# Kernel optimization log

Hardware: AMD Instinct MI355X
Metric: run time of the kernel (lower is better)

## Reference

```python
import jax, jax.numpy as jnp
import numpy as np

B, F, S, P, E, H = 64, 32, 512, 96, 8, 2048
TOP_K = 2
ALPHA = 10.0
ENT_EPS = 1e-8
CV_EPS = 1e-10


def setup_inputs() -> dict:
    key = jax.random.key(0)
    ks = jax.random.split(key, 8)
    s = 0.02
    return {
        "x": jax.random.normal(ks[0], (B, F, S), dtype=jnp.float32),
        "time_embedding": jax.random.normal(ks[1], (B, F, S), dtype=jnp.float32),
        "Wg": jax.random.normal(ks[2], (S, E), dtype=jnp.float32) * s,
        "bg": jnp.zeros((E,), dtype=jnp.float32),
        "W1": jax.random.normal(ks[3], (E, S, H), dtype=jnp.float32) * s,
        "b1": jnp.zeros((E, H), dtype=jnp.float32),
        "W2": jax.random.normal(ks[4], (E, H, P), dtype=jnp.float32) * s,
        "b2": jnp.zeros((E, P), dtype=jnp.float32),
    }


def _gates(tf, Wg, bg):
    # tf: [F, B, S] -> logits [F, B, E]
    logits = jnp.einsum('fbs,se->fbe', tf, Wg) + bg
    # kthvalue(x, E - top_k + 1) = (E - top_k)-th entry (0-based) of ascending sort = k-th largest
    kth = jnp.sort(logits, axis=-1)[..., E - TOP_K]  # [F, B]
    mask = logits < kth[..., None]
    sm = jax.nn.softmax(logits, axis=-1)
    dec = jnp.where(mask, ALPHA * jnp.log(sm + 1.0), ALPHA * (jnp.exp(sm) - 1.0))
    return jax.nn.softmax(dec, axis=-1)  # [F, B, E]


def reference(x, time_embedding, Wg, bg, W1, b1, W2, b2):
    xf = jnp.transpose(x, (1, 0, 2))               # [F, B, S]
    tf = jnp.transpose(time_embedding, (1, 0, 2))  # [F, B, S]
    gates = _gates(tf, Wg, bg)                     # [F, B, E]

    # all experts on all features (eval mode: dropout = identity)
    h = jax.nn.gelu(jnp.einsum('fbs,esh->febh', xf, W1) + b1[None, :, None, :], approximate=False)
    eo = jnp.einsum('febh,ehp->febp', h, W2) + b2[None, :, None, :]  # [F, E, B, P]
    out = jnp.einsum('fbe,febp->fbp', gates, eo)   # gated weighted sum
    output = jnp.transpose(out, (1, 0, 2))         # [B, F, P]

    # selector loss: cv_squared of importance = gates.sum(batch) expanded over pred_len
    gsum = gates.sum(axis=1)                       # [F, E]
    imp = jnp.broadcast_to(gsum[..., None], (F, E, P)).reshape(F, E * P)
    cv = jnp.var(imp, axis=1, ddof=1) / (jnp.mean(imp, axis=1) ** 2 + CV_EPS)
    selector_loss = jnp.sum(cv)                    # loss_coef = 1.0

    # entropy loss: importance1 = gates.mean(batch) expanded over pred_len
    gmean = gates.mean(axis=1)                     # [F, E]
    imp1 = jnp.broadcast_to(gmean[..., None], (F, E, P))
    entropy_loss = jnp.sum((-imp1 * jnp.log(imp1 + ENT_EPS)).mean(axis=(1, 2)))

    return output, selector_loss, entropy_loss
```

## Files before the change

### kernel.cpp

```cpp
#include <hip/hip_runtime.h>
#include <math.h>

#define B_ 64
#define F_ 32
#define S_ 512
#define P_ 96
#define E_ 8
#define H_ 2048
#define M_ 2048

#define BM 128
#define BH 128
#define BK 64
#define ZSPLIT 4
#define HPZ (H_ / ZSPLIT)
#define NHT (HPZ / BH)
#define NKC (S_ / BK)
#define HPITCH 136

typedef __bf16 bf16x8 __attribute__((ext_vector_type(8)));
typedef __bf16 bf16x4 __attribute__((ext_vector_type(4)));
typedef float f32x4 __attribute__((ext_vector_type(4)));

#define MFMA16(a, b, c) __builtin_amdgcn_mfma_f32_16x16x32_bf16((a), (b), (c), 0, 0, 0)

#define GLL16(gp, lp) __builtin_amdgcn_global_load_lds(                     \
    (const __attribute__((address_space(1))) void*)(gp),                    \
    (__attribute__((address_space(3))) void*)(lp), 16, 0, 0)

__device__ __forceinline__ float fast_gelu(float x) {
  float e = __builtin_amdgcn_exp2f(-2.45546696f * x);
  return x * __builtin_amdgcn_rcpf(1.0f + e);
}

#define PREP_GRID 3584

__global__ __launch_bounds__(256) void k_prep(const float* __restrict__ x,
                                              const float* __restrict__ te,
                                              const float* __restrict__ Wg,
                                              const float* __restrict__ bg,
                                              const float* __restrict__ W1,
                                              const float* __restrict__ W2,
                                              __bf16* __restrict__ xbf,
                                              __bf16* __restrict__ w1t,
                                              __bf16* __restrict__ w2t,
                                              float* __restrict__ gates) {
  __shared__ float tile[64 * 65];
  const int blk = blockIdx.x;
  const int tid = threadIdx.x;

  if (blk < 2048) {
    int e = blk >> 8, tt = blk & 255;
    int si = tt >> 5, hi = tt & 31;
    const float* src = W1 + (size_t)e * S_ * H_ + (size_t)(si * 64) * H_ + hi * 64;
    {
      int row = tid >> 2;
      int cb = (tid & 3) * 16;
#pragma unroll
      for (int k = 0; k < 4; ++k) {
        f32x4 v = *(const f32x4*)(src + (size_t)row * H_ + cb + k * 4);
#pragma unroll
        for (int u = 0; u < 4; ++u) tile[row * 65 + cb + k * 4 + u] = v[u];
      }
    }
    __syncthreads();
    {
      int h = tid >> 2;
      int sb = (tid & 3) * 16;
      __bf16* dst = w1t + (size_t)e * H_ * S_ + (size_t)(hi * 64 + h) * S_ + si * 64 + sb;
      bf16x8 o0, o1;
#pragma unroll
      for (int k = 0; k < 8; ++k) o0[k] = (__bf16)tile[(sb + k) * 65 + h];
#pragma unroll
      for (int k = 0; k < 8; ++k) o1[k] = (__bf16)tile[(sb + 8 + k) * 65 + h];
      *(bf16x8*)dst = o0;
      *(bf16x8*)(dst + 8) = o1;
    }
    return;
  }
  if (blk < 2560) {
    int t = blk - 2048;
    int e = t >> 6, hi = (t >> 1) & 31, ph = t & 1;
    const float* src = W2 + (size_t)e * H_ * P_ + (size_t)(hi * 64) * P_ + ph * 48;
    {
      int h = tid & 63;
      int seg = tid >> 6;
#pragma unroll
      for (int k = 0; k < 3; ++k) {
        f32x4 v = *(const f32x4*)(src + (size_t)h * P_ + seg * 12 + k * 4);
#pragma unroll
        for (int u = 0; u < 4; ++u) tile[h * 49 + seg * 12 + k * 4 + u] = v[u];
      }
    }
    __syncthreads();
    if (tid < 192) {
      int p = tid >> 2;
      int hb = (tid & 3) * 16;
      __bf16* dst = w2t + (size_t)e * P_ * H_ + (size_t)(ph * 48 + p) * H_ + hi * 64 + hb;
      bf16x8 o0, o1;
#pragma unroll
      for (int k = 0; k < 8; ++k) o0[k] = (__bf16)tile[(hb + k) * 49 + p];
#pragma unroll
      for (int k = 0; k < 8; ++k) o1[k] = (__bf16)tile[(hb + 8 + k) * 49 + p];
      *(bf16x8*)dst = o0;
      *(bf16x8*)(dst + 8) = o1;
    }
    return;
  }
  if (blk < 3072) {
    size_t i = (size_t)(blk - 2560) * 2048 + (size_t)tid * 8;
#pragma unroll
    for (int k = 0; k < 2; ++k) {
      f32x4 v = *(const f32x4*)(x + i + k * 4);
      bf16x4 o = {(__bf16)v[0], (__bf16)v[1], (__bf16)v[2], (__bf16)v[3]};
      *(bf16x4*)(xbf + i + k * 4) = o;
    }
    return;
  }
  int wave = tid >> 6, lane = tid & 63;
  int m = (blk - 3072) * 4 + wave;
  const float* trow = te + (size_t)m * S_;
  float acc[E_];
#pragma unroll
  for (int e = 0; e < E_; ++e) acc[e] = 0.f;
  for (int s = lane; s < S_; s += 64) {
    float t = trow[s];
    const f32x4* wgr = (const f32x4*)(Wg + s * E_);
    f32x4 a = wgr[0], b = wgr[1];
    acc[0] += t * a[0]; acc[1] += t * a[1]; acc[2] += t * a[2]; acc[3] += t * a[3];
    acc[4] += t * b[0]; acc[5] += t * b[1]; acc[6] += t * b[2]; acc[7] += t * b[3];
  }
#pragma unroll
  for (int e = 0; e < E_; ++e) {
#pragma unroll
    for (int off = 32; off > 0; off >>= 1) acc[e] += __shfl_xor(acc[e], off, 64);
  }
  if (lane == 0) {
    float lg[E_];
    float m1 = -3.4e38f, m2 = -3.4e38f;
#pragma unroll
    for (int e = 0; e < E_; ++e) {
      float v = acc[e] + bg[e];
      lg[e] = v;
      if (v > m1) { m2 = m1; m1 = v; }
      else if (v > m2) { m2 = v; }
    }
    float den = 0.f, sm[E_];
#pragma unroll
    for (int e = 0; e < E_; ++e) { sm[e] = expf(lg[e] - m1); den += sm[e]; }
    float inv = 1.f / den;
    float dmax = -3.4e38f, dec[E_];
#pragma unroll
    for (int e = 0; e < E_; ++e) {
      float p = sm[e] * inv;
      float d = (lg[e] < m2) ? (10.f * logf(p + 1.f)) : (10.f * (expf(p) - 1.f));
      dec[e] = d;
      dmax = fmaxf(dmax, d);
    }
    float dden = 0.f;
#pragma unroll
    for (int e = 0; e < E_; ++e) { dec[e] = expf(dec[e] - dmax); dden += dec[e]; }
    float dinv = 1.f / dden;
#pragma unroll
    for (int e = 0; e < E_; ++e) gates[m * E_ + e] = dec[e] * dinv;
  }
}

__global__ __launch_bounds__(256, 2) void k_experts(
    const __bf16* __restrict__ xbf,
    const __bf16* __restrict__ w1t,
    const __bf16* __restrict__ w2t,
    const float* __restrict__ b1,
    const float* __restrict__ b2,
    const float* __restrict__ gates,
    float* __restrict__ out)
{
  __shared__ __align__(16) __bf16 W1s[BH * BK];
  __shared__ __align__(16) __bf16 Xs[BM * BK];
  __shared__ __align__(16) __bf16 Hs[BM * HPITCH];

  const int tid = threadIdx.x;

  if (blockIdx.z == ZSPLIT) {
    if (blockIdx.x != 0 || blockIdx.y != 0) return;
    float* gsum = (float*)&Hs[0];
    float* cvs  = gsum + F_ * E_;
    float* ents = cvs + F_;
    int f = tid >> 3, e = tid & 7;
    float s = 0.f;
    for (int b = 0; b < B_; ++b) s += gates[(size_t)(b * F_ + f) * E_ + e];
    gsum[f * E_ + e] = s;
    __syncthreads();
    if (tid < F_) {
      float mean = 0.f;
#pragma unroll
      for (int k = 0; k < E_; ++k) mean += gsum[tid * E_ + k];
      mean *= (1.f / E_);
      float ss = 0.f;
#pragma unroll
      for (int k = 0; k < E_; ++k) { float d = gsum[tid * E_ + k] - mean; ss += d * d; }
      float var = (float)P_ * ss / (float)(E_ * P_ - 1);
      cvs[tid] = var / (mean * mean + 1e-10f);
      float ent = 0.f;
#pragma unroll
      for (int k = 0; k < E_; ++k) { float g = gsum[tid * E_ + k] * (1.f / B_); ent += -g * logf(g + 1e-8f); }
      ents[tid] = ent * (1.f / E_);
    }
    __syncthreads();
    if (tid == 0) {
      float a = 0.f, b = 0.f;
      for (int k = 0; k < F_; ++k) { a += cvs[k]; b += ents[k]; }
      out[(size_t)M_ * P_ + 0] = a;
      out[(size_t)M_ * P_ + 1] = b;
    }
    return;
  }

  const int wave = tid >> 6, lane = tid & 63;
  const int l15 = lane & 15, quad = lane >> 4;
  const int e = blockIdx.x;
  const int m0 = blockIdx.y * BM;
  const int hz = blockIdx.z * HPZ;

  const int sg = lane & 7;
  const int srl = lane >> 3;
  const int gcol = ((sg ^ srl) * 8);

  const __bf16* xg = xbf + (size_t)(m0 + wave * 8 + srl) * S_ + gcol;
  const __bf16* w1base = w1t + ((size_t)e * H_ + hz + wave * 8 + srl) * S_ + gcol;
  const __bf16* w2z = w2t + (size_t)e * P_ * H_ + hz;

  const int hq = (wave >> 1) * 64;
  const int mq = (wave & 1) * 64;
  const int w32 = wave * 32;

  const f32x4 fz = {0.f, 0.f, 0.f, 0.f};
  f32x4 acc2[2][6];
#pragma unroll
  for (int rt = 0; rt < 2; ++rt)
#pragma unroll
    for (int j = 0; j < 6; ++j) acc2[rt][j] = fz;

  for (int ht = 0; ht < NHT; ++ht) {
    const __bf16* w1g = w1base + (size_t)(ht * BH) * S_;
    f32x4 acc1[4][4];
#pragma unroll
    for (int i = 0; i < 4; ++i)
#pragma unroll
      for (int j = 0; j < 4; ++j) acc1[i][j] = fz;

    for (int kc = 0; kc < NKC; ++kc) {
#pragma unroll
      for (int p = 0; p < 4; ++p) {
        GLL16(w1g + (size_t)(p * 32) * S_ + kc * BK, &W1s[(p * 32 + wave * 8) * BK]);
        GLL16(xg  + (size_t)(p * 32) * S_ + kc * BK, &Xs[(p * 32 + wave * 8) * BK]);
      }
      __syncthreads();
#pragma unroll
      for (int kk = 0; kk < 2; ++kk) {
        bf16x8 a[4], b[4];
#pragma unroll
        for (int i = 0; i < 4; ++i) {
          int r = hq + i * 16 + l15;
          int g = kk * 4 + quad;
          a[i] = *(const bf16x8*)&W1s[r * BK + ((g ^ (r & 7)) * 8)];
        }
#pragma unroll
        for (int j = 0; j < 4; ++j) {
          int r = mq + j * 16 + l15;
          int g = kk * 4 + quad;
          b[j] = *(const bf16x8*)&Xs[r * BK + ((g ^ (r & 7)) * 8)];
        }
#pragma unroll
        for (int i = 0; i < 4; ++i)
#pragma unroll
          for (int j = 0; j < 4; ++j)
            acc1[i][j] = MFMA16(a[i], b[j], acc1[i][j]);
      }
      __syncthreads();
    }

    {
      const float* b1w = b1 + (size_t)e * H_ + hz + ht * BH + hq;
#pragma unroll
      for (int i = 0; i < 4; ++i) {
        f32x4 bv = *(const f32x4*)(b1w + i * 16 + quad * 4);
#pragma unroll
        for (int j = 0; j < 4; ++j) {
          bf16x4 hv;
#pragma unroll
          for (int r = 0; r < 4; ++r)
            hv[r] = (__bf16)fast_gelu(acc1[i][j][r] + bv[r]);
          *(bf16x4*)&Hs[(mq + j * 16 + l15) * HPITCH + hq + i * 16 + quad * 4] = hv;
        }
      }
    }
    __syncthreads();

    {
      const __bf16* w2c = w2z + ht * BH;
#pragma unroll
      for (int kk = 0; kk < 4; ++kk) {
        bf16x8 a0 = *(const bf16x8*)&Hs[(w32 + l15) * HPITCH + kk * 32 + quad * 8];
        bf16x8 a1 = *(const bf16x8*)&Hs[(w32 + 16 + l15) * HPITCH + kk * 32 + quad * 8];
#pragma unroll
        for (int j = 0; j < 6; ++j) {
          bf16x8 b = *(const bf16x8*)(w2c + (size_t)(j * 16 + l15) * H_ + kk * 32 + quad * 8);
          acc2[0][j] = MFMA16(a0, b, acc2[0][j]);
          acc2[1][j] = MFMA16(a1, b, acc2[1][j]);
        }
      }
    }
  }

#pragma unroll
  for (int rt = 0; rt < 2; ++rt) {
#pragma unroll
    for (int r = 0; r < 4; ++r) {
      int m = m0 + w32 + rt * 16 + quad * 4 + r;
      float g = gates[m * E_ + e];
#pragma unroll
      for (int j = 0; j < 6; ++j) {
        int col = j * 16 + l15;
        float v = acc2[rt][j][r];
        if (blockIdx.z == 0) v += b2[e * P_ + col];
        atomicAdd(&out[(size_t)m * P_ + col], g * v);
      }
    }
  }
}

extern "C" void kernel_launch(void* const* d_in, const int* in_sizes, int n_in,
                              void* d_out, int out_size, void* d_ws, size_t ws_size,
                              hipStream_t stream) {
  const float* x  = (const float*)d_in[0];
  const float* te = (const float*)d_in[1];
  const float* Wg = (const float*)d_in[2];
  const float* bg = (const float*)d_in[3];
  const float* W1 = (const float*)d_in[4];
  const float* b1 = (const float*)d_in[5];
  const float* W2 = (const float*)d_in[6];
  const float* b2 = (const float*)d_in[7];
  float* out = (float*)d_out;

  char* ws = (char*)d_ws;
  float* gates = (float*)ws;
  __bf16* xbf  = (__bf16*)(ws + 65536);
  __bf16* w1t  = (__bf16*)(ws + 65536 + 2097152);
  __bf16* w2t  = (__bf16*)(ws + 65536 + 2097152 + 16777216);

  hipMemsetAsync(d_out, 0, (size_t)out_size * sizeof(float), stream);
  k_prep<<<PREP_GRID, 256, 0, stream>>>(x, te, Wg, bg, W1, W2, xbf, w1t, w2t, gates);
  k_experts<<<dim3(E_, M_ / BM, ZSPLIT + 1), 256, 0, stream>>>(xbf, w1t, w2t, b1, b2, gates, out);
}
```

Baseline: 194.1 us.

## Double-buffer expert GEMM stages, stage W2 in LDS, fold output zeroing into prep

The expert kernel now uses 512-thread blocks with double-buffered W1/X LDS tiles. The next k-chunk loads while the current one computes, and the second GEMM for the previous h-tile overlaps the first chunk of the next. W2 tiles are staged into swizzled LDS instead of being read directly from global memory, and the H split drops from 4 to 2 to halve atomic traffic. The separate memset is replaced by extra zeroing blocks in the prep kernel, removing one launch. The trade-off is fewer blocks, higher LDS use per block and more serialized h-tiles per block.

```diff
diff --git a/kernel.cpp b/kernel.cpp
--- a/kernel.cpp
+++ b/kernel.cpp
@@ -12,7 +12,7 @@
 #define BM 128
 #define BH 128
 #define BK 64
-#define ZSPLIT 4
+#define ZSPLIT 2
 #define HPZ (H_ / ZSPLIT)
 #define NHT (HPZ / BH)
 #define NKC (S_ / BK)
@@ -33,7 +33,7 @@
   return x * __builtin_amdgcn_rcpf(1.0f + e);
 }
 
-#define PREP_GRID 3584
+#define PREP_GRID 3776
 
 __global__ __launch_bounds__(256) void k_prep(const float* __restrict__ x,
                                               const float* __restrict__ te,
@@ -44,7 +44,8 @@
                                               __bf16* __restrict__ xbf,
                                               __bf16* __restrict__ w1t,
                                               __bf16* __restrict__ w2t,
-                                              float* __restrict__ gates) {
+                                              float* __restrict__ gates,
+                                              float* __restrict__ out) {
   __shared__ float tile[64 * 65];
   const int blk = blockIdx.x;
   const int tid = threadIdx.x;
@@ -117,56 +118,64 @@
     }
     return;
   }
-  int wave = tid >> 6, lane = tid & 63;
-  int m = (blk - 3072) * 4 + wave;
-  const float* trow = te + (size_t)m * S_;
-  float acc[E_];
-#pragma unroll
-  for (int e = 0; e < E_; ++e) acc[e] = 0.f;
-  for (int s = lane; s < S_; s += 64) {
-    float t = trow[s];
-    const f32x4* wgr = (const f32x4*)(Wg + s * E_);
-    f32x4 a = wgr[0], b = wgr[1];
-    acc[0] += t * a[0]; acc[1] += t * a[1]; acc[2] += t * a[2]; acc[3] += t * a[3];
-    acc[4] += t * b[0]; acc[5] += t * b[1]; acc[6] += t * b[2]; acc[7] += t * b[3];
-  }
-#pragma unroll
-  for (int e = 0; e < E_; ++e) {
-#pragma unroll
-    for (int off = 32; off > 0; off >>= 1) acc[e] += __shfl_xor(acc[e], off, 64);
-  }
-  if (lane == 0) {
-    float lg[E_];
-    float m1 = -3.4e38f, m2 = -3.4e38f;
+  if (blk < 3584) {
+    int wave = tid >> 6, lane = tid & 63;
+    int m = (blk - 3072) * 4 + wave;
+    const float* trow = te + (size_t)m * S_;
+    float acc[E_];
+#pragma unroll
+    for (int e = 0; e < E_; ++e) acc[e] = 0.f;
+    for (int s = lane; s < S_; s += 64) {
+      float t = trow[s];
+      const f32x4* wgr = (const f32x4*)(Wg + s * E_);
+      f32x4 a = wgr[0], b = wgr[1];
+      acc[0] += t * a[0]; acc[1] += t * a[1]; acc[2] += t * a[2]; acc[3] += t * a[3];
+      acc[4] += t * b[0]; acc[5] += t * b[1]; acc[6] += t * b[2]; acc[7] += t * b[3];
+    }
 #pragma unroll
     for (int e = 0; e < E_; ++e) {
-      float v = acc[e] + bg[e];
-      lg[e] = v;
-      if (v > m1) { m2 = m1; m1 = v; }
-      else if (v > m2) { m2 = v; }
-    }
-    float den = 0.f, sm[E_];
-#pragma unroll
-    for (int e = 0; e < E_; ++e) { sm[e] = expf(lg[e] - m1); den += sm[e]; }
-    float inv = 1.f / den;
-    float dmax = -3.4e38f, dec[E_];
-#pragma unroll
-    for (int e = 0; e < E_; ++e) {
-      float p = sm[e] * inv;
-      float d = (lg[e] < m2) ? (10.f * logf(p + 1.f)) : (10.f * (expf(p) - 1.f));
-      dec[e] = d;
-      dmax = fmaxf(dmax, d);
-    }
-    float dden = 0.f;
-#pragma unroll
-    for (int e = 0; e < E_; ++e) { dec[e] = expf(dec[e] - dmax); dden += dec[e]; }
-    float dinv = 1.f / dden;
-#pragma unroll
-    for (int e = 0; e < E_; ++e) gates[m * E_ + e] = dec[e] * dinv;
+#pragma unroll
+      for (int off = 32; off > 0; off >>= 1) acc[e] += __shfl_xor(acc[e], off, 64);
+    }
+    if (lane == 0) {
+      float lg[E_];
+      float m1 = -3.4e38f, m2 = -3.4e38f;
+#pragma unroll
+      for (int e = 0; e < E_; ++e) {
+        float v = acc[e] + bg[e];
+        lg[e] = v;
+        if (v > m1) { m2 = m1; m1 = v; }
+        else if (v > m2) { m2 = v; }
+      }
+      float den = 0.f, sm[E_];
+#pragma unroll
+      for (int e = 0; e < E_; ++e) { sm[e] = expf(lg[e] - m1); den += sm[e]; }
+      float inv = 1.f / den;
+      float dmax = -3.4e38f, dec[E_];
+#pragma unroll
+      for (int e = 0; e < E_; ++e) {
+        float p = sm[e] * inv;
+        float d = (lg[e] < m2) ? (10.f * logf(p + 1.f)) : (10.f * (expf(p) - 1.f));
+        dec[e] = d;
+        dmax = fmaxf(dmax, d);
+      }
+      float dden = 0.f;
+#pragma unroll
+      for (int e = 0; e < E_; ++e) { dec[e] = expf(dec[e] - dmax); dden += dec[e]; }
+      float dinv = 1.f / dden;
+#pragma unroll
+      for (int e = 0; e < E_; ++e) gates[m * E_ + e] = dec[e] * dinv;
+    }
+    return;
+  }
+  {
+    size_t i = (size_t)(blk - 3584) * 1024 + (size_t)tid * 4;
+    f32x4 z4 = {0.f, 0.f, 0.f, 0.f};
+    *(f32x4*)(out + i) = z4;
   }
 }
 
-__global__ __launch_bounds__(256, 2) void k_experts(
+__global__ __launch_bounds__(512, 2) void k_experts(
     const __bf16* __restrict__ xbf,
     const __bf16* __restrict__ w1t,
     const __bf16* __restrict__ w2t,
@@ -175,8 +184,9 @@
     const float* __restrict__ gates,
     float* __restrict__ out)
 {
-  __shared__ __align__(16) __bf16 W1s[BH * BK];
-  __shared__ __align__(16) __bf16 Xs[BM * BK];
+  __shared__ __align__(16) __bf16 W1s[2][BH * BK];
+  __shared__ __align__(16) __bf16 Xs[2][BM * BK];
+  __shared__ __align__(16) __bf16 W2s[P_ * BH];
   __shared__ __align__(16) __bf16 Hs[BM * HPITCH];
 
   const int tid = threadIdx.x;
@@ -186,10 +196,12 @@
     float* gsum = (float*)&Hs[0];
     float* cvs  = gsum + F_ * E_;
     float* ents = cvs + F_;
-    int f = tid >> 3, e = tid & 7;
-    float s = 0.f;
-    for (int b = 0; b < B_; ++b) s += gates[(size_t)(b * F_ + f) * E_ + e];
-    gsum[f * E_ + e] = s;
+    if (tid < 256) {
+      int f = tid >> 3, ee = tid & 7;
+      float s = 0.f;
+      for (int b = 0; b < B_; ++b) s += gates[(size_t)(b * F_ + f) * E_ + ee];
+      gsum[f * E_ + ee] = s;
+    }
     __syncthreads();
     if (tid < F_) {
       float mean = 0.f;
@@ -226,106 +238,127 @@
   const int srl = lane >> 3;
   const int gcol = ((sg ^ srl) * 8);
 
-  const __bf16* xg = xbf + (size_t)(m0 + wave * 8 + srl) * S_ + gcol;
-  const __bf16* w1base = w1t + ((size_t)e * H_ + hz + wave * 8 + srl) * S_ + gcol;
+  const __bf16* w1base = w1t + ((size_t)e * H_ + hz + wave * 16 + srl) * S_ + gcol;
+  const __bf16* xg = xbf + (size_t)(m0 + wave * 16 + srl) * S_ + gcol;
   const __bf16* w2z = w2t + (size_t)e * P_ * H_ + hz;
 
-  const int hq = (wave >> 1) * 64;
-  const int mq = (wave & 1) * 64;
-  const int w32 = wave * 32;
+  const int hq = (wave & 1) * 64;
+  const int mq = (wave >> 1) * 32;
+  const int w16 = wave * 16;
 
   const f32x4 fz = {0.f, 0.f, 0.f, 0.f};
-  f32x4 acc2[2][6];
-#pragma unroll
-  for (int rt = 0; rt < 2; ++rt)
-#pragma unroll
-    for (int j = 0; j < 6; ++j) acc2[rt][j] = fz;
+  f32x4 acc1[4][2];
+  f32x4 acc2[6];
+#pragma unroll
+  for (int j = 0; j < 6; ++j) acc2[j] = fz;
+
+  auto STAGE = [&](int ht_, int kc_, int b) {
+    const __bf16* w1p = w1base + (size_t)(ht_ * BH) * S_ + kc_ * BK;
+    const __bf16* xp  = xg + kc_ * BK;
+#pragma unroll
+    for (int p = 0; p < 2; ++p) {
+      GLL16(w1p + (size_t)(p * 8) * S_, &W1s[b][(wave * 16 + p * 8) * BK]);
+      GLL16(xp  + (size_t)(p * 8) * S_, &Xs[b][(wave * 16 + p * 8) * BK]);
+    }
+  };
+
+  auto STAGEW2 = [&](int ht_) {
+#pragma unroll
+    for (int p = 0; p < 3; ++p) {
+      int r2 = wave * 12 + p * 4 + quad;
+      GLL16(w2z + (size_t)r2 * H_ + ht_ * BH + ((l15 ^ (r2 & 7)) * 8),
+            &W2s[(wave * 12 + p * 4) * BH]);
+    }
+  };
+
+  auto COMPUTE = [&](int b) {
+#pragma unroll
+    for (int kk = 0; kk < 2; ++kk) {
+      bf16x8 af[4], bx[2];
+#pragma unroll
+      for (int i = 0; i < 4; ++i) {
+        int r = hq + i * 16 + l15;
+        af[i] = *(const bf16x8*)&W1s[b][r * BK + (((kk * 4 + quad) ^ (r & 7)) * 8)];
+      }
+#pragma unroll
+      for (int j = 0; j < 2; ++j) {
+        int r = mq + j * 16 + l15;
+        bx[j] = *(const bf16x8*)&Xs[b][r * BK + (((kk * 4 + quad) ^ (r & 7)) * 8)];
+      }
+#pragma unroll
+      for (int i = 0; i < 4; ++i)
+#pragma unroll
+        for (int j = 0; j < 2; ++j)
+          acc1[i][j] = MFMA16(af[i], bx[j], acc1[i][j]);
+    }
+  };
+
+  auto GEMM2 = [&]() {
+#pragma unroll
+    for (int kk = 0; kk < 4; ++kk) {
+      bf16x8 a = *(const bf16x8*)&Hs[(w16 + l15) * HPITCH + kk * 32 + quad * 8];
+#pragma unroll
+      for (int j = 0; j < 6; ++j) {
+        bf16x8 bb = *(const bf16x8*)&W2s[(j * 16 + l15) * BH + (((kk * 4 + quad) ^ (l15 & 7)) * 8)];
+        acc2[j] = MFMA16(a, bb, acc2[j]);
+      }
+    }
+  };
+
+  auto GELU = [&](int ht_) {
+    const float* b1w = b1 + (size_t)e * H_ + hz + ht_ * BH + hq;
+#pragma unroll
+    for (int i = 0; i < 4; ++i) {
+      f32x4 bv = *(const f32x4*)(b1w + i * 16 + quad * 4);
+#pragma unroll
+      for (int j = 0; j < 2; ++j) {
+        bf16x4 hv;
+#pragma unroll
+        for (int r = 0; r < 4; ++r)
+          hv[r] = (__bf16)fast_gelu(acc1[i][j][r] + bv[r]);
+        *(bf16x4*)&Hs[(mq + j * 16 + l15) * HPITCH + hq + i * 16 + quad * 4] = hv;
+      }
+    }
+  };
+
+  STAGE(0, 0, 0);
+  __syncthreads();
 
   for (int ht = 0; ht < NHT; ++ht) {
-    const __bf16* w1g = w1base + (size_t)(ht * BH) * S_;
-    f32x4 acc1[4][4];
 #pragma unroll
     for (int i = 0; i < 4; ++i)
 #pragma unroll
-      for (int j = 0; j < 4; ++j) acc1[i][j] = fz;
-
+      for (int j = 0; j < 2; ++j) acc1[i][j] = fz;
+
+    int bsel = 0;
+#pragma unroll
     for (int kc = 0; kc < NKC; ++kc) {
-#pragma unroll
-      for (int p = 0; p < 4; ++p) {
-        GLL16(w1g + (size_t)(p * 32) * S_ + kc * BK, &W1s[(p * 32 + wave * 8) * BK]);
-        GLL16(xg  + (size_t)(p * 32) * S_ + kc * BK, &Xs[(p * 32 + wave * 8) * BK]);
-      }
+      if (kc < NKC - 1) {
+        STAGE(ht, kc + 1, bsel ^ 1);
+      } else {
+        if (ht < NHT - 1) STAGE(ht + 1, 0, bsel ^ 1);
+        STAGEW2(ht);
+      }
+      if (kc == 0 && ht > 0) GEMM2();
+      COMPUTE(bsel);
       __syncthreads();
-#pragma unroll
-      for (int kk = 0; kk < 2; ++kk) {
-        bf16x8 a[4], b[4];
-#pragma unroll
-        for (int i = 0; i < 4; ++i) {
-          int r = hq + i * 16 + l15;
-          int g = kk * 4 + quad;
-          a[i] = *(const bf16x8*)&W1s[r * BK + ((g ^ (r & 7)) * 8)];
-        }
-#pragma unroll
-        for (int j = 0; j < 4; ++j) {
-          int r = mq + j * 16 + l15;
-          int g = kk * 4 + quad;
-          b[j] = *(const bf16x8*)&Xs[r * BK + ((g ^ (r & 7)) * 8)];
-        }
-#pragma unroll
-        for (int i = 0; i < 4; ++i)
-#pragma unroll
-          for (int j = 0; j < 4; ++j)
-            acc1[i][j] = MFMA16(a[i], b[j], acc1[i][j]);
-      }
-      __syncthreads();
-    }
-
-    {
-      const float* b1w = b1 + (size_t)e * H_ + hz + ht * BH + hq;
-#pragma unroll
-      for (int i = 0; i < 4; ++i) {
-        f32x4 bv = *(const f32x4*)(b1w + i * 16 + quad * 4);
-#pragma unroll
-        for (int j = 0; j < 4; ++j) {
-          bf16x4 hv;
-#pragma unroll
-          for (int r = 0; r < 4; ++r)
-            hv[r] = (__bf16)fast_gelu(acc1[i][j][r] + bv[r]);
-          *(bf16x4*)&Hs[(mq + j * 16 + l15) * HPITCH + hq + i * 16 + quad * 4] = hv;
-        }
-      }
-    }
-    __syncthreads();
-
-    {
-      const __bf16* w2c = w2z + ht * BH;
-#pragma unroll
-      for (int kk = 0; kk < 4; ++kk) {
-        bf16x8 a0 = *(const bf16x8*)&Hs[(w32 + l15) * HPITCH + kk * 32 + quad * 8];
-        bf16x8 a1 = *(const bf16x8*)&Hs[(w32 + 16 + l15) * HPITCH + kk * 32 + quad * 8];
-#pragma unroll
-        for (int j = 0; j < 6; ++j) {
-          bf16x8 b = *(const bf16x8*)(w2c + (size_t)(j * 16 + l15) * H_ + kk * 32 + quad * 8);
-          acc2[0][j] = MFMA16(a0, b, acc2[0][j]);
-          acc2[1][j] = MFMA16(a1, b, acc2[1][j]);
-        }
-      }
-    }
-  }
-
-#pragma unroll
-  for (int rt = 0; rt < 2; ++rt) {
-#pragma unroll
-    for (int r = 0; r < 4; ++r) {
-      int m = m0 + w32 + rt * 16 + quad * 4 + r;
-      float g = gates[m * E_ + e];
-#pragma unroll
-      for (int j = 0; j < 6; ++j) {
-        int col = j * 16 + l15;
-        float v = acc2[rt][j][r];
-        if (blockIdx.z == 0) v += b2[e * P_ + col];
-        atomicAdd(&out[(size_t)m * P_ + col], g * v);
-      }
+      bsel ^= 1;
+    }
+    GELU(ht);
+    __syncthreads();
+  }
+  GEMM2();
+
+#pragma unroll
+  for (int r = 0; r < 4; ++r) {
+    int m = m0 + w16 + quad * 4 + r;
+    float g = gates[m * E_ + e];
+#pragma unroll
+    for (int j = 0; j < 6; ++j) {
+      int col = j * 16 + l15;
+      float v = acc2[j][r];
+      if (blockIdx.z == 0) v += b2[e * P_ + col];
+      atomicAdd(&out[(size_t)m * P_ + col], g * v);
     }
   }
 }
@@ -349,7 +382,6 @@
   __bf16* w1t  = (__bf16*)(ws + 65536 + 2097152);
   __bf16* w2t  = (__bf16*)(ws + 65536 + 2097152 + 16777216);
 
-  hipMemsetAsync(d_out, 0, (size_t)out_size * sizeof(float), stream);
-  k_prep<<<PREP_GRID, 256, 0, stream>>>(x, te, Wg, bg, W1, W2, xbf, w1t, w2t, gates);
-  k_experts<<<dim3(E_, M_ / BM, ZSPLIT + 1), 256, 0, stream>>>(xbf, w1t, w2t, b1, b2, gates, out);
+  k_prep<<<PREP_GRID, 256, 0, stream>>>(x, te, Wg, bg, W1, W2, xbf, w1t, w2t, gates, out);
+  k_experts<<<dim3(E_, M_ / BM, ZSPLIT + 1), 512, 0, stream>>>(xbf, w1t, w2t, b1, b2, gates, out);
 }
```

Result: faster. 185.7 us (-4.3%).
